# Kernel tuning notes

Hardware: AMD Instinct MI355X
Metric: run time of the kernel (lower is better)

## Reference

```python
import jax, jax.numpy as jnp
import numpy as np

B, N, D, H, L, K, V = 2, 2048, 512, 8, 4, 32, 256
HD = D // H
MOD = 4294967296.0
SCALE = 1.0 / np.sqrt(HD)


def _ln(x, g, b):
    m = x.mean(-1, keepdims=True)
    v = ((x - m) ** 2).mean(-1, keepdims=True)
    return (x - m) * jax.lax.rsqrt(v + 1e-5) * g + b


def _expmap0(v, c):
    sc = jnp.sqrt(c)
    vn = jnp.maximum(jnp.linalg.norm(v, axis=-1, keepdims=True), 1e-8)
    return jnp.tanh(sc * vn) * v / (sc * vn)


def _knn_poincare(pos, c):
    xx = jnp.sum(pos ** 2, -1)                                    # [N]
    d2 = jnp.maximum(xx[:, None] + xx[None, :] - 2.0 * pos @ pos.T, 0.0)
    denom = (1.0 - c * xx)[:, None] * (1.0 - c * xx)[None, :] + 1e-8
    arg = jnp.maximum(1.0 + 2.0 * c * d2 / denom, 1.0)
    dist = jnp.arccosh(arg) / jnp.sqrt(c)                         # [N,N]
    neg_d, idx = jax.lax.top_k(-dist, K)                          # smallest-k
    return -neg_d, idx                                            # [N,K],[N,K]


def _forward(hashes, indices, emb, hash_proj, Wb, bb, log_c, pos_tangent,
             Wq, bq, Wk, bk, Wv, bv, Wo, bo, W1, b1, W2, b2,
             g1, be1, g2, be2, log_tau, Wout, bout):
    c = jnp.exp(log_c)
    char = emb[indices]                                           # [B,N,D]
    he = (hashes[..., None].astype(jnp.float32) / MOD) @ hash_proj  # [B,N,D]
    x = jnp.concatenate([char, he], -1) @ Wb + bb                 # [B,N,D]

    # kNN structure computed under no_grad in the original
    pos = _expmap0(jax.lax.stop_gradient(pos_tangent), jax.lax.stop_gradient(c))
    attn_dists, idx = _knn_poincare(pos, jax.lax.stop_gradient(c))  # shared over batch

    for i in range(L):
        xn = _ln(x, g1[i], be1[i])
        q = (xn @ Wq[i] + bq[i]).reshape(B, N, H, HD).transpose(0, 2, 1, 3)
        k = (xn @ Wk[i] + bk[i]).reshape(B, N, H, HD).transpose(0, 2, 1, 3)
        v = (xn @ Wv[i] + bv[i]).reshape(B, N, H, HD).transpose(0, 2, 1, 3)
        kg = k[:, :, idx, :]                                      # [B,H,N,K,HD]
        vg = v[:, :, idx, :]
        fs = jnp.einsum('bhnd,bhnkd->bhnk', q, kg) * SCALE
        gs = -attn_dists[None, None] / (jnp.exp(log_tau[i]) + 1e-8)
        p = jax.nn.softmax(fs + gs, axis=-1)                      # [B,H,N,K]
        ao = jnp.einsum('bhnk,bhnkd->bhnd', p, vg)
        ao = ao.transpose(0, 2, 1, 3).reshape(B, N, D)
        x = x + ao @ Wo[i] + bo[i]
        xn2 = _ln(x, g2[i], be2[i])
        x = x + jax.nn.gelu(xn2 @ W1[i] + b1[i], approximate=False) @ W2[i] + b2[i]

    return x[:, -1, :] @ Wout + bout                              # [B,V]


def setup_inputs():
    key = jax.random.key(0)
    ks = jax.random.split(key, 20)
    rn = lambda k, s, sc=0.02: jax.random.normal(k, s, jnp.float32) * sc
    z = lambda s: jnp.zeros(s, jnp.float32)
    o = lambda s: jnp.ones(s, jnp.float32)
    return {
        'hashes': jax.random.randint(ks[0], (B, N), 0, 1000000),
        'indices': jax.random.randint(ks[1], (B, N), 0, V),
        'emb': rn(ks[2], (V, D)),
        'hash_proj': rn(ks[3], (1, D)),
        'Wb': rn(ks[4], (2 * D, D)),
        'bb': z((D,)),
        'log_c': jnp.array(0.0, jnp.float32),
        'pos_tangent': rn(ks[5], (N, D)),
        'Wq': rn(ks[6], (L, D, D)), 'bq': z((L, D)),
        'Wk': rn(ks[7], (L, D, D)), 'bk': z((L, D)),
        'Wv': rn(ks[8], (L, D, D)), 'bv': z((L, D)),
        'Wo': rn(ks[9], (L, D, D)), 'bo': z((L, D)),
        'W1': rn(ks[10], (L, D, 4 * D)), 'b1': z((L, 4 * D)),
        'W2': rn(ks[11], (L, 4 * D, D)), 'b2': z((L, D)),
        'g1': o((L, D)), 'be1': z((L, D)),
        'g2': o((L, D)), 'be2': z((L, D)),
        'log_tau': z((L,)),
        'Wout': rn(ks[12], (D, V)), 'bout': z((V,)),
    }


def reference(hashes, indices, emb, hash_proj, Wb, bb, log_c, pos_tangent,
              Wq, bq, Wk, bk, Wv, bv, Wo, bo, W1, b1, W2, b2,
              g1, be1, g2, be2, log_tau, Wout, bout):
    return _forward(hashes, indices, emb, hash_proj, Wb, bb, log_c, pos_tangent,
                    Wq, bq, Wk, bk, Wv, bv, Wo, bo, W1, b1, W2, b2,
                    g1, be1, g2, be2, log_tau, Wout, bout)
```

## Files before the change

### kernel.cpp

```cpp
#include <hip/hip_runtime.h>
#include <hip/hip_bf16.h>
#include <math.h>

#define Bb 2
#define Nn 2048
#define Dd 512
#define Hh 8
#define Ll 4
#define Kk 32
#define Vv 256
#define HDh 64
#define Mrows (Bb*Nn)

static constexpr float SCALE_QK = 0.125f;
static constexpr float INV_MOD = 1.0f / 4294967296.0f;

typedef _Float16 f16;
typedef _Float16 f16x8 __attribute__((ext_vector_type(8)));
typedef _Float16 f16x4 __attribute__((ext_vector_type(4)));
typedef _Float16 f16x2 __attribute__((ext_vector_type(2)));
typedef float f32x4 __attribute__((ext_vector_type(4)));
typedef unsigned long long u64;

#define AS_GLOBAL(p) ((const __attribute__((address_space(1))) void*)(p))
#define AS_LDS(p)    ((__attribute__((address_space(3))) void*)(p))
__device__ __forceinline__ void gload16(const f16* g, f16* l) {
    __builtin_amdgcn_global_load_lds(AS_GLOBAL(g), AS_LDS(l), 16, 0, 0);
}

__global__ void scal_kernel(const float* __restrict__ log_c,
                            const float* __restrict__ log_tau,
                            float* __restrict__ scal) {
    int t = threadIdx.x;
    if (t == 0) {
        float c = expf(log_c[0]);
        scal[0] = c;
        scal[1] = sqrtf(c);
    }
    if (t < Ll) scal[2 + t] = 1.0f / (expf(log_tau[t]) + 1e-8f);
}

__global__ __launch_bounds__(256)
void hvec_part_kernel(const float* __restrict__ hash_proj,
                      const float* __restrict__ Wb,
                      float* __restrict__ part) {
    const int b = blockIdx.x;
    const int t = threadIdx.x;
    float a0 = 0.f, a1 = 0.f;
#pragma unroll
    for (int i = 0; i < 16; i++) {
        int kx = b * 16 + i;
        float hp = hash_proj[kx];
        const float* wr = Wb + (size_t)(Dd + kx) * Dd;
        a0 = fmaf(hp, wr[t], a0);
        a1 = fmaf(hp, wr[t + 256], a1);
    }
    part[b * Dd + t]       = a0;
    part[b * Dd + t + 256] = a1;
}
__global__ __launch_bounds__(256)
void hvec_red_kernel(const float* __restrict__ part, float* __restrict__ hvec) {
    const int n = blockIdx.x * 256 + threadIdx.x;
    float acc = 0.f;
#pragma unroll
    for (int b = 0; b < 32; b++) acc += part[b * Dd + n];
    hvec[n] = acc;
}

__global__ void conv_kernel(const float* __restrict__ src, f16* __restrict__ dst, int n) {
    int i = blockIdx.x * 256 + threadIdx.x;
    if (i < n) dst[i] = (f16)src[i];
}

__global__ void pack_bias_kernel(const float* __restrict__ bq, const float* __restrict__ bk,
                                 const float* __restrict__ bv, float* __restrict__ bqkv) {
    int t = blockIdx.x * 256 + threadIdx.x;
    int l = t / 1536, r = t % 1536;
    const float* src = (r < 512) ? bq : ((r < 1024) ? bk : bv);
    bqkv[t] = src[l * 512 + (r & 511)];
}

__global__ __launch_bounds__(256)
void trans_kernel(const float* __restrict__ src, f16* __restrict__ dst,
                  int K, int N, long sStride, long dStride) {
    __shared__ float tile[32][33];
    const float* s = src + blockIdx.z * sStride;
    f16* d = dst + blockIdx.z * dStride;
    int k0 = blockIdx.y * 32, n0 = blockIdx.x * 32;
    int tx = threadIdx.x & 31, ty = threadIdx.x >> 5;
#pragma unroll
    for (int i = 0; i < 32; i += 8)
        tile[ty + i][tx] = s[(long)(k0 + ty + i) * N + n0 + tx];
    __syncthreads();
#pragma unroll
    for (int i = 0; i < 32; i += 8)
        d[(long)(n0 + ty + i) * K + k0 + tx] = (f16)tile[tx][ty + i];
}

__global__ __launch_bounds__(256)
void trans4_kernel(const float* __restrict__ Wq, const float* __restrict__ Wk,
                   const float* __restrict__ Wv, const float* __restrict__ Wo,
                   f16* __restrict__ Wqkvt, f16* __restrict__ Wot) {
    __shared__ float tile[32][33];
    const int which = blockIdx.z >> 2, l = blockIdx.z & 3;
    const float* s;
    f16* d;
    switch (which) {
        case 0: s = Wq + (size_t)l * 262144; d = Wqkvt + (size_t)l * 786432;          break;
        case 1: s = Wk + (size_t)l * 262144; d = Wqkvt + (size_t)l * 786432 + 262144; break;
        case 2: s = Wv + (size_t)l * 262144; d = Wqkvt + (size_t)l * 786432 + 524288; break;
        default:s = Wo + (size_t)l * 262144; d = Wot   + (size_t)l * 262144;          break;
    }
    int k0 = blockIdx.y * 32, n0 = blockIdx.x * 32;
    int tx = threadIdx.x & 31, ty = threadIdx.x >> 5;
#pragma unroll
    for (int i = 0; i < 32; i += 8)
        tile[ty + i][tx] = s[(long)(k0 + ty + i) * 512 + n0 + tx];
    __syncthreads();
#pragma unroll
    for (int i = 0; i < 32; i += 8)
        d[(long)(n0 + ty + i) * 512 + k0 + tx] = (f16)tile[tx][ty + i];
}

template<int TN, bool GATHER, bool RANK1, bool GELU, bool RES, bool OUT16>
__global__ __launch_bounds__(256)
void mgemm(const f16* __restrict__ A, const f16* __restrict__ Wt,
           const float* __restrict__ bias,
           const int* __restrict__ gidx,
           const int* __restrict__ hashes, const float* __restrict__ hvec,
           const float* __restrict__ resid,
           void* __restrict__ Cout, int M, int N, int K) {
    constexpr int TM  = 64;
    constexpr int WRN = (TN == 64) ? 2 : 1;
    constexpr int WCN = 4 / WRN;
    constexpr int WRE = TM / WRN;
    constexpr int NIT = WRE / 16;
    constexpr int ACH = TM * 8;
    constexpr int BCH = TN * 8;
    constexpr int NCH = ACH + BCH;
    constexpr int NCHT = NCH / 256;
    constexpr int NBUF = (TN == 64) ? 3 : 2;
    __shared__ __align__(16) f16 sm[NBUF][NCH * 8];
    const int t = threadIdx.x;
    const int lane = t & 63;
    const int w = t >> 6;
    const int wr = w / WCN, wc = w % WCN;
    const int i0 = blockIdx.y * TM, j0 = blockIdx.x * TN;

    const f16* gsrc[NCHT];
#pragma unroll
    for (int q = 0; q < NCHT; q++) {
        int c = t + q * 256;
        if (c < ACH) {
            int m = c >> 3, kb = (c & 7) ^ (m & 7);
            long row = GATHER ? (long)gidx[i0 + m] : (long)(i0 + m);
            gsrc[q] = A + row * K + kb * 8;
        } else {
            int cc = c - ACH;
            int n = cc >> 3, kb = (cc & 7) ^ (n & 7);
            gsrc[q] = Wt + (long)(j0 + n) * K + kb * 8;
        }
    }

    f32x4 acc[NIT][2];
#pragma unroll
    for (int i = 0; i < NIT; i++)
#pragma unroll
        for (int j = 0; j < 2; j++) acc[i][j] = (f32x4){0.f, 0.f, 0.f, 0.f};

    auto compute = [&](const f16* rbuf) {
#pragma unroll
        for (int kh = 0; kh < 2; kh++) {
            f16x8 af[NIT], bf[2];
#pragma unroll
            for (int i = 0; i < NIT; i++) {
                int m = wr * WRE + i * 16 + (lane & 15);
                int sl = m * 8 + ((kh * 4 + (lane >> 4)) ^ (m & 7));
                af[i] = *(const f16x8*)(rbuf + sl * 8);
            }
#pragma unroll
            for (int j = 0; j < 2; j++) {
                int n = wc * 32 + j * 16 + (lane & 15);
                int sl = ACH + n * 8 + ((kh * 4 + (lane >> 4)) ^ (n & 7));
                bf[j] = *(const f16x8*)(rbuf + sl * 8);
            }
#pragma unroll
            for (int i = 0; i < NIT; i++)
#pragma unroll
                for (int j = 0; j < 2; j++)
                    acc[i][j] = __builtin_amdgcn_mfma_f32_16x16x32_f16(af[i], bf[j], acc[i][j], 0, 0, 0);
        }
    };

    if constexpr (TN == 64) {
        static_assert(NCHT == 4, "vmcnt immediates assume NCHT==4");
        const int T = K >> 6;
#pragma unroll
        for (int q = 0; q < NCHT; q++) gload16(gsrc[q],      &sm[0][(t + q * 256) * 8]);
#pragma unroll
        for (int q = 0; q < NCHT; q++) gload16(gsrc[q] + 64, &sm[1][(t + q * 256) * 8]);
        f16 *bA = sm[0], *bB = sm[1], *bC = sm[2];
        for (int tt = 0; tt < T - 1; ++tt) {
            asm volatile("s_waitcnt vmcnt(4)" ::: "memory");
            __syncthreads();
            if (tt + 2 < T) {
                const int kt2 = (tt + 2) << 6;
#pragma unroll
                for (int q = 0; q < NCHT; q++)
                    gload16(gsrc[q] + kt2, bC + (t + q * 256) * 8);
            }
            compute(bA);
            f16* tmp = bA; bA = bB; bB = bC; bC = tmp;
        }
        asm volatile("s_waitcnt vmcnt(0)" ::: "memory");
        __syncthreads();
        compute(bA);
    } else {
#pragma unroll
        for (int q = 0; q < NCHT; q++)
            gload16(gsrc[q], &sm[0][(t + q * 256) * 8]);
        auto step = [&](int kt, const f16* rbuf, f16* wbuf) {
            asm volatile("s_waitcnt vmcnt(0)" ::: "memory");
            __syncthreads();
            if (kt + 64 < K) {
#pragma unroll
                for (int q = 0; q < NCHT; q++)
                    gload16(gsrc[q] + kt + 64, wbuf + (t + q * 256) * 8);
            }
            compute(rbuf);
        };
        for (int kt = 0; kt < K; kt += 128) {
            step(kt,      sm[0], sm[1]);
            step(kt + 64, sm[1], sm[0]);
        }
    }

    float* Cf = (float*)Cout;
    f16*   Ch = (f16*)Cout;
#pragma unroll
    for (int i = 0; i < NIT; i++) {
        int rbase = i0 + wr * WRE + i * 16 + ((lane >> 4) << 2);
#pragma unroll
        for (int v = 0; v < 4; v++) {
            int row = rbase + v;
            float hterm = RANK1 ? (float)hashes[row] * INV_MOD : 0.f;
#pragma unroll
            for (int j = 0; j < 2; j++) {
                int col = j0 + wc * 32 + j * 16 + (lane & 15);
                float val = acc[i][j][v] + bias[col];
                if (RANK1) val += hterm * hvec[col];
                if (GELU)  val = 0.5f * val * (1.f + erff(val * 0.7071067811865475f));
                if (RES)   val += resid[(long)row * N + col];
                if (OUT16) Ch[(long)row * N + col] = (f16)val;
                else       Cf[(long)row * N + col] = val;
            }
        }
    }
}

__global__ __launch_bounds__(256)
void mdist_kernel(const f16* __restrict__ poshl, const float* __restrict__ xx,
                  const float* __restrict__ scal, float* __restrict__ dist) {
    constexpr int TM = 64, TN = 64;
    constexpr int ACH = TM * 8, BCH = TN * 8, NCH = ACH + BCH;
    constexpr int NCHT = NCH / 256;
    constexpr int KK = 1024;
    __shared__ __align__(16) f16 sm[3][NCH * 8];
    const int t = threadIdx.x;
    const int lane = t & 63;
    const int w = t >> 6;
    const int wr = w >> 1, wc = w & 1;
    const int i0 = blockIdx.y * TM, j0 = blockIdx.x * TN;

    const f16* gsrc[NCHT];
#pragma unroll
    for (int q = 0; q < NCHT; q++) {
        int c = t + q * 256;
        if (c < ACH) {
            int m = c >> 3, kb = (c & 7) ^ (m & 7);
            gsrc[q] = poshl + (long)(i0 + m) * KK + kb * 8;
        } else {
            int cc = c - ACH;
            int n = cc >> 3, kb = (cc & 7) ^ (n & 7);
            gsrc[q] = poshl + (long)(j0 + n) * KK + kb * 8;
        }
    }

    f32x4 acc[2][2];
#pragma unroll
    for (int i = 0; i < 2; i++)
#pragma unroll
        for (int j = 0; j < 2; j++) acc[i][j] = (f32x4){0.f, 0.f, 0.f, 0.f};

    auto compute = [&](const f16* rbuf) {
#pragma unroll
        for (int kh = 0; kh < 2; kh++) {
            f16x8 af[2], bf[2];
#pragma unroll
            for (int i = 0; i < 2; i++) {
                int m = wr * 32 + i * 16 + (lane & 15);
                int sl = m * 8 + ((kh * 4 + (lane >> 4)) ^ (m & 7));
                af[i] = *(const f16x8*)(rbuf + sl * 8);
            }
#pragma unroll
            for (int j = 0; j < 2; j++) {
                int n = wc * 32 + j * 16 + (lane & 15);
                int sl = ACH + n * 8 + ((kh * 4 + (lane >> 4)) ^ (n & 7));
                bf[j] = *(const f16x8*)(rbuf + sl * 8);
            }
#pragma unroll
            for (int i = 0; i < 2; i++)
#pragma unroll
                for (int j = 0; j < 2; j++)
                    acc[i][j] = __builtin_amdgcn_mfma_f32_16x16x32_f16(af[i], bf[j], acc[i][j], 0, 0, 0);
        }
    };

#pragma unroll
    for (int q = 0; q < NCHT; q++) gload16(gsrc[q],      &sm[0][(t + q * 256) * 8]);
#pragma unroll
    for (int q = 0; q < NCHT; q++) gload16(gsrc[q] + 64, &sm[1][(t + q * 256) * 8]);
    f16 *bA = sm[0], *bB = sm[1], *bC = sm[2];
    constexpr int T = KK >> 6;
    for (int tt = 0; tt < T - 1; ++tt) {
        asm volatile("s_waitcnt vmcnt(4)" ::: "memory");
        __syncthreads();
        if (tt + 2 < T) {
            const int kt2 = (tt + 2) << 6;
#pragma unroll
            for (int q = 0; q < NCHT; q++)
                gload16(gsrc[q] + kt2, bC + (t + q * 256) * 8);
        }
        compute(bA);
        f16* tmp = bA; bA = bB; bB = bC; bC = tmp;
    }
    asm volatile("s_waitcnt vmcnt(0)" ::: "memory");
    __syncthreads();
    compute(bA);

    const float c = scal[0];
#pragma unroll
    for (int i = 0; i < 2; i++) {
        int rbase = i0 + wr * 32 + i * 16 + ((lane >> 4) << 2);
#pragma unroll
        for (int v = 0; v < 4; v++) {
            int row = rbase + v;
            float xi = xx[row];
#pragma unroll
            for (int j = 0; j < 2; j++) {
                int col = j0 + wc * 32 + j * 16 + (lane & 15);
                float xj = xx[col];
                float d2 = fmaxf(xi + xj - 2.f * acc[i][j][v], 0.f);
                float denom = (1.f - c * xi) * (1.f - c * xj) + 1e-8f;
                float arg = fmaxf(1.f + 2.f * c * d2 / denom, 1.f);
                dist[(long)row * Nn + col] = arg;
            }
        }
    }
}

__global__ __launch_bounds__(256)
void ln_kernel(const float* __restrict__ x, const float* __restrict__ g,
               const float* __restrict__ be, f16* __restrict__ xn) {
    const int row = blockIdx.x * 4 + (threadIdx.x >> 6);
    const int t = threadIdx.x & 63;
    const float4* xr = (const float4*)(x + (size_t)row * Dd);
    float4 v0 = xr[t], v1 = xr[t + 64];
    float s = v0.x + v0.y + v0.z + v0.w + v1.x + v1.y + v1.z + v1.w;
#pragma unroll
    for (int off = 32; off; off >>= 1) s += __shfl_xor(s, off, 64);
    float mean = s * (1.f / Dd);
    float d0x = v0.x - mean, d0y = v0.y - mean, d0z = v0.z - mean, d0w = v0.w - mean;
    float d1x = v1.x - mean, d1y = v1.y - mean, d1z = v1.z - mean, d1w = v1.w - mean;
    float q = d0x*d0x + d0y*d0y + d0z*d0z + d0w*d0w
            + d1x*d1x + d1y*d1y + d1z*d1z + d1w*d1w;
#pragma unroll
    for (int off = 32; off; off >>= 1) q += __shfl_xor(q, off, 64);
    float rstd = rsqrtf(q * (1.f / Dd) + 1e-5f);
    float4 g0 = ((const float4*)g)[t], g1v = ((const float4*)g)[t + 64];
    float4 b0 = ((const float4*)be)[t], b1v = ((const float4*)be)[t + 64];
    f16* xo = xn + (size_t)row * Dd;
    f16x4 o0, o1;
    o0[0] = (f16)(d0x * rstd * g0.x + b0.x);
    o0[1] = (f16)(d0y * rstd * g0.y + b0.y);
    o0[2] = (f16)(d0z * rstd * g0.z + b0.z);
    o0[3] = (f16)(d0w * rstd * g0.w + b0.w);
    o1[0] = (f16)(d1x * rstd * g1v.x + b1v.x);
    o1[1] = (f16)(d1y * rstd * g1v.y + b1v.y);
    o1[2] = (f16)(d1z * rstd * g1v.z + b1v.z);
    o1[3] = (f16)(d1w * rstd * g1v.w + b1v.w);
    *(f16x4*)(xo + t * 4)         = o0;
    *(f16x4*)(xo + (t + 64) * 4)  = o1;
}

__global__ __launch_bounds__(256)
void expmap_kernel(const float* __restrict__ vt, const float* __restrict__ scal,
                   f16* __restrict__ poshl, float* __restrict__ xx) {
    __shared__ float red[256];
    const int row = blockIdx.x, t = threadIdx.x;
    const float* vr = vt + (size_t)row * Dd;
    float v0 = vr[t], v1 = vr[t + 256];
    red[t] = v0 * v0 + v1 * v1;
    __syncthreads();
    for (int off = 128; off; off >>= 1) {
        if (t < off) red[t] += red[t + off];
        __syncthreads();
    }
    float total = red[0];
    float vn = fmaxf(sqrtf(total), 1e-8f);
    float sc = scal[1];
    float factor = tanhf(sc * vn) / (sc * vn);
    float p0 = factor * v0, p1 = factor * v1;
    f16 h0 = (f16)p0, h1 = (f16)p1;
    f16* pr = poshl + (size_t)row * 1024;
    pr[t]             = h0;
    pr[t + 256]       = h1;
    pr[512 + t]       = (f16)(p0 - (float)h0);
    pr[512 + t + 256] = (f16)(p1 - (float)h1);
    if (t == 0) xx[row] = factor * factor * total;
}

__global__ __launch_bounds__(256)
void topk_kernel(const float* __restrict__ dist, const float* __restrict__ scal,
                 float* __restrict__ outd, int* __restrict__ outi) {
    __shared__ unsigned wred[4];
    __shared__ unsigned bc;
    __shared__ __align__(8) u64 buf[128];
    const int t = threadIdx.x;
    const int w = t >> 6;
    const int n = blockIdx.x;
    const float sqc = scal[1];
    const uint4* dr = (const uint4*)(dist + (size_t)n * Nn);

    uint4 va = dr[t * 2];
    uint4 vb = dr[t * 2 + 1];
    unsigned k[8] = {va.x, va.y, va.z, va.w, vb.x, vb.y, vb.z, vb.w};
    const int g0 = t * 8;

    unsigned lo = 0x3F800000u;
    unsigned hi = 0x7F800001u;
    unsigned chi = 2048u;
    while (chi > 96u && (hi - lo) > 1u) {
        unsigned mid = lo + ((hi - lo) >> 1);
        int c = 0;
#pragma unroll
        for (int j = 0; j < 8; j++) c += (k[j] < mid) ? 1 : 0;
#pragma unroll
        for (int off = 32; off; off >>= 1) c += __shfl_xor(c, off, 64);
        __syncthreads();
        if ((t & 63) == 0) wred[w] = (unsigned)c;
        __syncthreads();
        unsigned ct = wred[0] + wred[1] + wred[2] + wred[3];
        if (ct >= 32u) { hi = mid; chi = ct; } else { lo = mid; }
    }

    if (chi <= 96u) {
        if (t == 0) bc = 0u;
        __syncthreads();
#pragma unroll
        for (int j = 0; j < 8; j++) {
            if (k[j] < hi) {
                unsigned s = atomicAdd(&bc, 1u);
                buf[s] = ((u64)k[j] << 11) | (u64)(unsigned)(g0 + j);
            }
        }
        __syncthreads();
        const int m = (int)chi;
        if (t < m) {
            u64 my = buf[t];
            int r = 0;
            for (int j = 0; j < m; j++) r += (buf[j] < my) ? 1 : 0;
            if (r < Kk) {
                float v = __uint_as_float((unsigned)(my >> 11));
                outd[n * Kk + r] = acoshf(v) / sqc;
                outi[n * Kk + r] = (int)(my & 2047u);
            }
        }
    } else {
        int c = 0;
#pragma unroll
        for (int j = 0; j < 8; j++) c += (k[j] < lo) ? 1 : 0;
#pragma unroll
        for (int off = 32; off; off >>= 1) c += __shfl_xor(c, off, 64);
        __syncthreads();
        if ((t & 63) == 0) wred[w] = (unsigned)c;
        if (t == 0) bc = 0u;
        __syncthreads();
        const int cless = (int)(wred[0] + wred[1] + wred[2] + wred[3]);
#pragma unroll
        for (int j = 0; j < 8; j++) {
            if (k[j] < lo) {
                unsigned s = atomicAdd(&bc, 1u);
                buf[s] = ((u64)k[j] << 11) | (u64)(unsigned)(g0 + j);
            }
        }
        __syncthreads();
        if (t < cless) {
            u64 my = buf[t];
            int r = 0;
            for (int j = 0; j < cless; j++) r += (buf[j] < my) ? 1 : 0;
            float v = __uint_as_float((unsigned)(my >> 11));
            outd[n * Kk + r] = acoshf(v) / sqc;
            outi[n * Kk + r] = (int)(my & 2047u);
        }
        const int need = Kk - cless;
        unsigned eqm = 0u;
#pragma unroll
        for (int j = 0; j < 8; j++) if (k[j] == lo) eqm |= (1u << j);
        const float dv = acoshf(__uint_as_float(lo)) / sqc;
        for (int s = 0; s < need; s++) {
            int mi = 0x7FFFFFFF;
#pragma unroll
            for (int j = 0; j < 8; j++)
                if (eqm & (1u << j)) mi = min(mi, g0 + j);
#pragma unroll
            for (int off = 32; off; off >>= 1) mi = min(mi, __shfl_xor(mi, off, 64));
            __syncthreads();
            if ((t & 63) == 0) wred[w] = (unsigned)mi;
            __syncthreads();
            int m4 = (int)min(min(wred[0], wred[1]), min(wred[2], wred[3]));
            int j = m4 - g0;
            if (j >= 0 && j < 8 && (eqm & (1u << j))) {
                eqm &= ~(1u << j);
                outd[n * Kk + cless + s] = dv;
                outi[n * Kk + cless + s] = m4;
            }
        }
    }
}

#define KSTR 520
__global__ __launch_bounds__(256)
void attn_kernel(const f16* __restrict__ qkv, const float* __restrict__ adist,
                 const int* __restrict__ aidx, const float* __restrict__ scal,
                 int layer, f16* __restrict__ ao) {
    __shared__ __align__(16) f16 ks[Kk * KSTR];
    __shared__ float ps[Hh][Kk];
    __shared__ int   sidx[Kk];
    const int t = threadIdx.x;
    const int b = blockIdx.x >> 11, n = blockIdx.x & (Nn - 1);
    const float inv_tau = scal[2 + layer];
    const int h = t >> 5, j = t & 31;

    if (t < Kk) sidx[t] = aidx[n * Kk + t];
#pragma unroll
    for (int q = 0; q < 8; q++) {
        int c = q * 256 + t;
        int jr = c >> 6, ci = c & 63;
        int row = aidx[n * Kk + jr];
        *(f16x8*)(ks + jr * KSTR + ci * 8) =
            *(const f16x8*)(qkv + (size_t)(b * Nn + row) * 1536 + 512 + ci * 8);
    }
    __syncthreads();

    const f16* qrow = qkv + (size_t)(b * Nn + n) * 1536 + h * HDh;
    float dot = 0.f;
#pragma unroll
    for (int i = 0; i < 8; i++) {
        f16x8 qa = *(const f16x8*)(qrow + i * 8);
        f16x8 ka = *(const f16x8*)(ks + j * KSTR + h * HDh + i * 8);
#pragma unroll
        for (int m = 0; m < 4; m++) {
            f16x2 qp = {qa[2 * m], qa[2 * m + 1]};
            f16x2 kp = {ka[2 * m], ka[2 * m + 1]};
            dot = __builtin_amdgcn_fdot2(qp, kp, dot, false);
        }
    }
    float s = dot * SCALE_QK - adist[n * Kk + j] * inv_tau;
    float mx = s;
#pragma unroll
    for (int off = 16; off; off >>= 1) mx = fmaxf(mx, __shfl_xor(mx, off, 64));
    float e = expf(s - mx);
    float sum = e;
#pragma unroll
    for (int off = 16; off; off >>= 1) sum += __shfl_xor(sum, off, 64);
    ps[h][j] = e / sum;
    __syncthreads();

    const int d2 = t & 31;
    const size_t voff = 1024 + (size_t)h * HDh + d2 * 2;
    float a0 = 0.f, a1 = 0.f;
#pragma unroll
    for (int jj = 0; jj < Kk; jj++) {
        float p = ps[h][jj];
        f16x2 vv = *(const f16x2*)(qkv + (size_t)(b * Nn + sidx[jj]) * 1536 + voff);
        a0 = fmaf(p, (float)vv[0], a0);
        a1 = fmaf(p, (float)vv[1], a1);
    }
    f16x2 outv; outv[0] = (f16)a0; outv[1] = (f16)a1;
    *(f16x2*)(ao + (size_t)(b * Nn + n) * Dd + h * HDh + d2 * 2) = outv;
}

__global__ __launch_bounds__(1024)
void out_kernel(const float* __restrict__ x, const float* __restrict__ Wout,
                const float* __restrict__ bout, float* __restrict__ out) {
    __shared__ float red[3][256];
    const int b = blockIdx.x;
    const int g = threadIdx.x >> 8, vc = threadIdx.x & 255;
    const float* xr = x + ((size_t)(b * Nn + (Nn - 1))) * Dd;
    float acc = 0.f;
    for (int d = g * 128; d < (g + 1) * 128; d++)
        acc = fmaf(xr[d], Wout[(size_t)d * Vv + vc], acc);
    if (g) red[g - 1][vc] = acc;
    __syncthreads();
    if (g == 0)
        out[b * Vv + vc] = acc + red[0][vc] + red[1][vc] + red[2][vc] + bout[vc];
}

static constexpr size_t X_OFF     = 0;
static constexpr size_t XN16_OFF  = 8388608;
static constexpr size_t QKV16_OFF = 12582912;
static constexpr size_t AO16_OFF  = 25165824;
static constexpr size_t H1_OFF    = 29360128;
static constexpr size_t AD_OFF    = 46137344;
static constexpr size_t AI_OFF    = 46399488;
static constexpr size_t SC_OFF    = 46661632;
static constexpr size_t HV_OFF    = 46661888;
static constexpr size_t XX_OFF    = 46663936;
static constexpr size_t BQKV_OFF  = 46672128;
static constexpr size_t EMB16_OFF = 46704896;
static constexpr size_t WBT_OFF   = 46967040;
static constexpr size_t WQKVT_OFF = 47491328;
static constexpr size_t WOT_OFF   = 53782784;
static constexpr size_t W1T_OFF   = 55879936;
static constexpr size_t W2T_OFF   = 64268544;
static constexpr size_t HP_OFF    = 72657152;

extern "C" void kernel_launch(void* const* d_in, const int* in_sizes, int n_in,
                              void* d_out, int out_size, void* d_ws, size_t ws_size,
                              hipStream_t stream) {
    (void)in_sizes; (void)n_in; (void)out_size; (void)ws_size;
    const int*   hashes    = (const int*)  d_in[0];
    const int*   indices   = (const int*)  d_in[1];
    const float* emb       = (const float*)d_in[2];
    const float* hash_proj = (const float*)d_in[3];
    const float* Wb        = (const float*)d_in[4];
    const float* bb        = (const float*)d_in[5];
    const float* log_c     = (const float*)d_in[6];
    const float* pos_t     = (const float*)d_in[7];
    const float* Wq        = (const float*)d_in[8];
    const float* bq        = (const float*)d_in[9];
    const float* Wk        = (const float*)d_in[10];
    const float* bk        = (const float*)d_in[11];
    const float* Wv        = (const float*)d_in[12];
    const float* bv        = (const float*)d_in[13];
    const float* Wo        = (const float*)d_in[14];
    const float* bo        = (const float*)d_in[15];
    const float* W1        = (const float*)d_in[16];
    const float* b1        = (const float*)d_in[17];
    const float* W2        = (const float*)d_in[18];
    const float* b2        = (const float*)d_in[19];
    const float* g1        = (const float*)d_in[20];
    const float* be1       = (const float*)d_in[21];
    const float* g2        = (const float*)d_in[22];
    const float* be2       = (const float*)d_in[23];
    const float* log_tau   = (const float*)d_in[24];
    const float* Wout      = (const float*)d_in[25];
    const float* bout      = (const float*)d_in[26];

    char* ws = (char*)d_ws;
    float* x      = (float*)(ws + X_OFF);
    f16*   xn16   = (f16*)  (ws + XN16_OFF);
    f16*   qkv16  = (f16*)  (ws + QKV16_OFF);
    f16*   ao16   = (f16*)  (ws + AO16_OFF);
    f16*   h1     = (f16*)  (ws + H1_OFF);
    float* adist  = (float*)(ws + AD_OFF);
    int*   aidx   = (int*)  (ws + AI_OFF);
    float* scal   = (float*)(ws + SC_OFF);
    float* hvec   = (float*)(ws + HV_OFF);
    float* xxb    = (float*)(ws + XX_OFF);
    float* bqkv   = (float*)(ws + BQKV_OFF);
    f16*   emb16  = (f16*)  (ws + EMB16_OFF);
    f16*   Wbt    = (f16*)  (ws + WBT_OFF);
    f16*   Wqkvt  = (f16*)  (ws + WQKVT_OFF);
    f16*   Wot    = (f16*)  (ws + WOT_OFF);
    f16*   W1t    = (f16*)  (ws + W1T_OFF);
    f16*   W2t    = (f16*)  (ws + W2T_OFF);
    float* hpart  = (float*)(ws + HP_OFF);
    f16*   poshl  = (f16*)  (ws + AO16_OFF);
    float* distb  = (float*)(ws + H1_OFF);

    scal_kernel<<<1, 64, 0, stream>>>(log_c, log_tau, scal);
    hvec_part_kernel<<<32, 256, 0, stream>>>(hash_proj, Wb, hpart);
    hvec_red_kernel<<<2, 256, 0, stream>>>(hpart, hvec);
    pack_bias_kernel<<<24, 256, 0, stream>>>(bq, bk, bv, bqkv);
    conv_kernel<<<(Vv * Dd + 255) / 256, 256, 0, stream>>>(emb, emb16, Vv * Dd);
    trans_kernel<<<dim3(16, 16, 1), 256, 0, stream>>>(Wb, Wbt, 512, 512, 0, 0);
    trans4_kernel<<<dim3(16, 16, 16), 256, 0, stream>>>(Wq, Wk, Wv, Wo, Wqkvt, Wot);
    trans_kernel<<<dim3(64, 16, Ll), 256, 0, stream>>>(W1, W1t, 512, 2048, 1048576, 1048576);
    trans_kernel<<<dim3(16, 64, Ll), 256, 0, stream>>>(W2, W2t, 2048, 512, 1048576, 1048576);

    mgemm<64, true, true, false, false, false><<<dim3(8, 64), 256, 0, stream>>>(
        emb16, Wbt, bb, indices, hashes, hvec, nullptr, x, Mrows, Dd, Dd);

    expmap_kernel<<<Nn, 256, 0, stream>>>(pos_t, scal, poshl, xxb);
    mdist_kernel<<<dim3(32, 32), 256, 0, stream>>>(poshl, xxb, scal, distb);
    topk_kernel<<<Nn, 256, 0, stream>>>(distb, scal, adist, aidx);

    for (int l = 0; l < Ll; l++) {
        ln_kernel<<<Mrows / 4, 256, 0, stream>>>(x, g1 + l * Dd, be1 + l * Dd, xn16);
        mgemm<128, false, false, false, false, true><<<dim3(12, 64), 256, 0, stream>>>(
            xn16, Wqkvt + (size_t)l * 786432, bqkv + l * 1536,
            nullptr, nullptr, nullptr, nullptr, qkv16, Mrows, 1536, Dd);
        attn_kernel<<<Bb * Nn, 256, 0, stream>>>(qkv16, adist, aidx, scal, l, ao16);
        mgemm<64, false, false, false, true, false><<<dim3(8, 64), 256, 0, stream>>>(
            ao16, Wot + (size_t)l * 262144, bo + l * Dd,
            nullptr, nullptr, nullptr, x, x, Mrows, Dd, Dd);
        ln_kernel<<<Mrows / 4, 256, 0, stream>>>(x, g2 + l * Dd, be2 + l * Dd, xn16);
        mgemm<128, false, false, true, false, true><<<dim3(16, 64), 256, 0, stream>>>(
            xn16, W1t + (size_t)l * 1048576, b1 + l * 4 * Dd,
            nullptr, nullptr, nullptr, nullptr, h1, Mrows, 4 * Dd, Dd);
        mgemm<64, false, false, false, true, false><<<dim3(8, 64), 256, 0, stream>>>(
            h1, W2t + (size_t)l * 1048576, b2 + l * Dd,
            nullptr, nullptr, nullptr, x, x, Mrows, Dd, 4 * Dd);
    }

    out_kernel<<<Bb, 1024, 0, stream>>>(x, Wout, bout, (float*)d_out);
}
```

Baseline: 583.8 us.

## Split-K the residual GEMMs with atomic accumulation and fuse prep kernels

The Wo and W2 GEMMs, which produce only 512 blocks each, now split K across 2 and 4 z-slices. Each slice atomically adds its partial sum into the residual buffer x, and only the lead slice adds the bias. This raises block-level parallelism on the many-CU GPU at the cost of float atomics, nondeterministic summation order, and a slower double-buffer path instead of the triple-buffer one. The scalar, bias-packing and embedding-conversion prep kernels are also merged into a single launch to cut launch overhead.

Result: slower. 705.2 us (+20.8%).

```diff
diff --git a/kernel.cpp b/kernel.cpp
--- a/kernel.cpp
+++ b/kernel.cpp
@@ -28,16 +28,25 @@
     __builtin_amdgcn_global_load_lds(AS_GLOBAL(g), AS_LDS(l), 16, 0, 0);
 }
 
-__global__ void scal_kernel(const float* __restrict__ log_c,
-                            const float* __restrict__ log_tau,
-                            float* __restrict__ scal) {
-    int t = threadIdx.x;
-    if (t == 0) {
+__global__ __launch_bounds__(256)
+void prep_kernel(const float* __restrict__ log_c, const float* __restrict__ log_tau,
+                 float* __restrict__ scal,
+                 const float* __restrict__ bq, const float* __restrict__ bk,
+                 const float* __restrict__ bv, float* __restrict__ bqkv,
+                 const float* __restrict__ emb, f16* __restrict__ emb16) {
+    int id = blockIdx.x * 256 + threadIdx.x;
+    if (id < Vv * Dd) emb16[id] = (f16)emb[id];
+    if (id < Ll * 1536) {
+        int l = id / 1536, r = id % 1536;
+        const float* src = (r < 512) ? bq : ((r < 1024) ? bk : bv);
+        bqkv[id] = src[l * 512 + (r & 511)];
+    }
+    if (id == 0) {
         float c = expf(log_c[0]);
         scal[0] = c;
         scal[1] = sqrtf(c);
     }
-    if (t < Ll) scal[2 + t] = 1.0f / (expf(log_tau[t]) + 1e-8f);
+    if (id < Ll) scal[2 + id] = 1.0f / (expf(log_tau[id]) + 1e-8f);
 }
 
 __global__ __launch_bounds__(256)
@@ -65,19 +74,6 @@
 #pragma unroll
     for (int b = 0; b < 32; b++) acc += part[b * Dd + n];
     hvec[n] = acc;
-}
-
-__global__ void conv_kernel(const float* __restrict__ src, f16* __restrict__ dst, int n) {
-    int i = blockIdx.x * 256 + threadIdx.x;
-    if (i < n) dst[i] = (f16)src[i];
-}
-
-__global__ void pack_bias_kernel(const float* __restrict__ bq, const float* __restrict__ bk,
-                                 const float* __restrict__ bv, float* __restrict__ bqkv) {
-    int t = blockIdx.x * 256 + threadIdx.x;
-    int l = t / 1536, r = t % 1536;
-    const float* src = (r < 512) ? bq : ((r < 1024) ? bk : bv);
-    bqkv[t] = src[l * 512 + (r & 511)];
 }
 
 __global__ __launch_bounds__(256)
@@ -122,7 +118,7 @@
         d[(long)(n0 + ty + i) * 512 + k0 + tx] = (f16)tile[tx][ty + i];
 }
 
-template<int TN, bool GATHER, bool RANK1, bool GELU, bool RES, bool OUT16>
+template<int TN, int SPLITK, bool GATHER, bool RANK1, bool GELU, bool RES, bool OUT16>
 __global__ __launch_bounds__(256)
 void mgemm(const f16* __restrict__ A, const f16* __restrict__ Wt,
            const float* __restrict__ bias,
@@ -130,6 +126,8 @@
            const int* __restrict__ hashes, const float* __restrict__ hvec,
            const float* __restrict__ resid,
            void* __restrict__ Cout, int M, int N, int K) {
+    static_assert(SPLITK == 1 || (TN == 64 && RES && !OUT16 && !RANK1 && !GELU && !GATHER),
+                  "split-K only for the f32 residual-accumulate sites");
     constexpr int TM  = 64;
     constexpr int WRN = (TN == 64) ? 2 : 1;
     constexpr int WCN = 4 / WRN;
@@ -139,13 +137,16 @@
     constexpr int BCH = TN * 8;
     constexpr int NCH = ACH + BCH;
     constexpr int NCHT = NCH / 256;
-    constexpr int NBUF = (TN == 64) ? 3 : 2;
+    constexpr int NBUF = (TN == 64 && SPLITK == 1) ? 3 : 2;
     __shared__ __align__(16) f16 sm[NBUF][NCH * 8];
     const int t = threadIdx.x;
     const int lane = t & 63;
     const int w = t >> 6;
     const int wr = w / WCN, wc = w % WCN;
     const int i0 = blockIdx.y * TM, j0 = blockIdx.x * TN;
+    const int Kslice = K / SPLITK;
+    const int k0 = (SPLITK > 1) ? (int)blockIdx.z * Kslice : 0;
+    const int klim = k0 + Kslice;
 
     const f16* gsrc[NCHT];
 #pragma unroll
@@ -192,7 +193,7 @@
         }
     };
 
-    if constexpr (TN == 64) {
+    if constexpr (TN == 64 && SPLITK == 1) {
         static_assert(NCHT == 4, "vmcnt immediates assume NCHT==4");
         const int T = K >> 6;
 #pragma unroll
@@ -218,18 +219,18 @@
     } else {
 #pragma unroll
         for (int q = 0; q < NCHT; q++)
-            gload16(gsrc[q], &sm[0][(t + q * 256) * 8]);
+            gload16(gsrc[q] + k0, &sm[0][(t + q * 256) * 8]);
         auto step = [&](int kt, const f16* rbuf, f16* wbuf) {
             asm volatile("s_waitcnt vmcnt(0)" ::: "memory");
             __syncthreads();
-            if (kt + 64 < K) {
+            if (kt + 64 < klim) {
 #pragma unroll
                 for (int q = 0; q < NCHT; q++)
                     gload16(gsrc[q] + kt + 64, wbuf + (t + q * 256) * 8);
             }
             compute(rbuf);
         };
-        for (int kt = 0; kt < K; kt += 128) {
+        for (int kt = k0; kt < klim; kt += 128) {
             step(kt,      sm[0], sm[1]);
             step(kt + 64, sm[1], sm[0]);
         }
@@ -237,6 +238,7 @@
 
     float* Cf = (float*)Cout;
     f16*   Ch = (f16*)Cout;
+    const bool lead = (SPLITK == 1) || (blockIdx.z == 0);
 #pragma unroll
     for (int i = 0; i < NIT; i++) {
         int rbase = i0 + wr * WRE + i * 16 + ((lane >> 4) << 2);
@@ -247,12 +249,17 @@
 #pragma unroll
             for (int j = 0; j < 2; j++) {
                 int col = j0 + wc * 32 + j * 16 + (lane & 15);
-                float val = acc[i][j][v] + bias[col];
-                if (RANK1) val += hterm * hvec[col];
-                if (GELU)  val = 0.5f * val * (1.f + erff(val * 0.7071067811865475f));
-                if (RES)   val += resid[(long)row * N + col];
-                if (OUT16) Ch[(long)row * N + col] = (f16)val;
-                else       Cf[(long)row * N + col] = val;
+                if constexpr (SPLITK > 1) {
+                    float val = acc[i][j][v] + (lead ? bias[col] : 0.f);
+                    atomicAdd(&Cf[(long)row * N + col], val);
+                } else {
+                    float val = acc[i][j][v] + bias[col];
+                    if (RANK1) val += hterm * hvec[col];
+                    if (GELU)  val = 0.5f * val * (1.f + erff(val * 0.7071067811865475f));
+                    if (RES)   val += resid[(long)row * N + col];
+                    if (OUT16) Ch[(long)row * N + col] = (f16)val;
+                    else       Cf[(long)row * N + col] = val;
+                }
             }
         }
     }
@@ -680,17 +687,15 @@
     f16*   poshl  = (f16*)  (ws + AO16_OFF);
     float* distb  = (float*)(ws + H1_OFF);
 
-    scal_kernel<<<1, 64, 0, stream>>>(log_c, log_tau, scal);
+    prep_kernel<<<512, 256, 0, stream>>>(log_c, log_tau, scal, bq, bk, bv, bqkv, emb, emb16);
     hvec_part_kernel<<<32, 256, 0, stream>>>(hash_proj, Wb, hpart);
     hvec_red_kernel<<<2, 256, 0, stream>>>(hpart, hvec);
-    pack_bias_kernel<<<24, 256, 0, stream>>>(bq, bk, bv, bqkv);
-    conv_kernel<<<(Vv * Dd + 255) / 256, 256, 0, stream>>>(emb, emb16, Vv * Dd);
     trans_kernel<<<dim3(16, 16, 1), 256, 0, stream>>>(Wb, Wbt, 512, 512, 0, 0);
     trans4_kernel<<<dim3(16, 16, 16), 256, 0, stream>>>(Wq, Wk, Wv, Wo, Wqkvt, Wot);
     trans_kernel<<<dim3(64, 16, Ll), 256, 0, stream>>>(W1, W1t, 512, 2048, 1048576, 1048576);
     trans_kernel<<<dim3(16, 64, Ll), 256, 0, stream>>>(W2, W2t, 2048, 512, 1048576, 1048576);
 
-    mgemm<64, true, true, false, false, false><<<dim3(8, 64), 256, 0, stream>>>(
+    mgemm<64, 1, true, true, false, false, false><<<dim3(8, 64), 256, 0, stream>>>(
         emb16, Wbt, bb, indices, hashes, hvec, nullptr, x, Mrows, Dd, Dd);
 
     expmap_kernel<<<Nn, 256, 0, stream>>>(pos_t, scal, poshl, xxb);
@@ -699,20 +704,20 @@
 
     for (int l = 0; l < Ll; l++) {
         ln_kernel<<<Mrows / 4, 256, 0, stream>>>(x, g1 + l * Dd, be1 + l * Dd, xn16);
-        mgemm<128, false, false, false, false, true><<<dim3(12, 64), 256, 0, stream>>>(
+        mgemm<128, 1, false, false, false, false, true><<<dim3(12, 64), 256, 0, stream>>>(
             xn16, Wqkvt + (size_t)l * 786432, bqkv + l * 1536,
             nullptr, nullptr, nullptr, nullptr, qkv16, Mrows, 1536, Dd);
         attn_kernel<<<Bb * Nn, 256, 0, stream>>>(qkv16, adist, aidx, scal, l, ao16);
-        mgemm<64, false, false, false, true, false><<<dim3(8, 64), 256, 0, stream>>>(
+        mgemm<64, 2, false, false, false, true, false><<<dim3(8, 64, 2), 256, 0, stream>>>(
             ao16, Wot + (size_t)l * 262144, bo + l * Dd,
-            nullptr, nullptr, nullptr, x, x, Mrows, Dd, Dd);
+            nullptr, nullptr, nullptr, nullptr, x, Mrows, Dd, Dd);
         ln_kernel<<<Mrows / 4, 256, 0, stream>>>(x, g2 + l * Dd, be2 + l * Dd, xn16);
-        mgemm<128, false, false, true, false, true><<<dim3(16, 64), 256, 0, stream>>>(
+        mgemm<128, 1, false, false, true, false, true><<<dim3(16, 64), 256, 0, stream>>>(
             xn16, W1t + (size_t)l * 1048576, b1 + l * 4 * Dd,
             nullptr, nullptr, nullptr, nullptr, h1, Mrows, 4 * Dd, Dd);
-        mgemm<64, false, false, false, true, false><<<dim3(8, 64), 256, 0, stream>>>(
+        mgemm<64, 4, false, false, false, true, false><<<dim3(8, 64, 4), 256, 0, stream>>>(
             h1, W2t + (size_t)l * 1048576, b2 + l * Dd,
-            nullptr, nullptr, nullptr, x, x, Mrows, Dd, 4 * Dd);
+            nullptr, nullptr, nullptr, nullptr, x, Mrows, Dd, 4 * Dd);
     }
 
     out_kernel<<<Bb, 1024, 0, stream>>>(x, Wout, bout, (float*)d_out);
```
